# Kernel optimization log

Hardware: AMD Instinct MI355X
Metric: run time of the kernel (lower is better)

## Reference

```python
import jax, jax.numpy as jnp
import numpy as np

L = 256
UP = 2
# ktype -> (rotations, ((pad_top,pad_bot),(pad_left,pad_right)), (b_row_off, b_col_off))
CONFIG = {
    'h': ([0, 2],        ((0, 0), (0, 1)), (0, 1)),
    'd': ([0, 1, 2, 3],  ((0, 1), (0, 1)), (1, 1)),
    'v': ([0, 2],        ((0, 1), (0, 0)), (1, 0)),
}


def setup_inputs() -> dict:
    key = jax.random.key(0)
    k0, k1, k2, k3 = jax.random.split(key, 4)
    img_lr = jax.random.randint(k0, (32, 1, 512, 512), 0, L, dtype=jnp.int32)
    h_weight = jax.random.normal(k1, (L * L, UP * UP), dtype=jnp.float32)
    d_weight = jax.random.normal(k2, (L * L, UP * UP), dtype=jnp.float32)
    v_weight = jax.random.normal(k3, (L * L, UP * UP), dtype=jnp.float32)
    return {"img_lr": img_lr, "h_weight": h_weight, "d_weight": d_weight, "v_weight": v_weight}


def reference(img_lr, h_weight, d_weight, v_weight):
    B, C, H0, W0 = img_lr.shape
    weights = {'h': h_weight, 'd': d_weight, 'v': v_weight}
    out = jnp.zeros((B, C, H0 * UP, W0 * UP), dtype=jnp.float32)
    for ktype in ('h', 'd', 'v'):
        rots, (ph, pw), (dr, dc) = CONFIG[ktype]
        w = weights[ktype].reshape(L * L, UP, UP)
        for r in rots:
            rot = jnp.rot90(img_lr, r, axes=(2, 3))
            H, W = rot.shape[2], rot.shape[3]
            padded = jnp.pad(rot, ((0, 0), (0, 0), ph, pw), mode='edge').astype(jnp.int32)
            img_a = padded[:, :, 0:H, 0:W]
            img_b = padded[:, :, dr:dr + H, dc:dc + W]
            # LUT gather: [B,C,H,W,UP,UP]
            tmp = w[img_a * L + img_b]
            # interleave subpixels: (B,C,H,uh,W,uw) -> (B,C,H*UP,W*UP)
            tmp = tmp.transpose(0, 1, 2, 4, 3, 5).reshape(B, C, H * UP, W * UP)
            out = out + jnp.rot90(tmp, (4 - r) % 4, axes=(2, 3))
    return out / 2.0
```

## Files before the change

### kernel.cpp

```cpp
#include <hip/hip_runtime.h>


typedef _Float16 h8 __attribute__((ext_vector_type(8)));
typedef _Float16 h4 __attribute__((ext_vector_type(4)));
typedef unsigned u32x2 __attribute__((ext_vector_type(2)));
typedef float    f32x4 __attribute__((ext_vector_type(4)));

#define P3_CURS(ws, i) (((unsigned*)(ws))[(size_t)(i) << 4])
#define P3_LUT16(ws)   ((h4*)((char*)(ws) + 0x100000))
#define P3_SMAP(ws)    ((unsigned*)((char*)(ws) + 0x280000))
#define P3_RECS(ws)    ((u32x2*)((char*)(ws) + 0x2280000))
#define P3_RES(ws)     ((h4*)((char*)(ws) + 0x8280000))
#define P3_AB(ws)      ((unsigned char*)((char*)(ws) + 0xE280000))
#define P3_NEED        0xEE80000ull
#define P3_CAP         12288u

__global__ __launch_bounds__(256) void p3_init(void* ws)
{
    for (int k = 0; k < 4; ++k) {
        int i = k * 256 + threadIdx.x;
        if (i < 1024) P3_CURS(ws, i) = (unsigned)i * P3_CAP;
    }
}

__global__ __launch_bounds__(256) void p2_lut16(
    const float4* __restrict__ wh,
    const float4* __restrict__ wv,
    const float4* __restrict__ wd,
    h4* __restrict__ lut16)
{
    int idx = blockIdx.x * 256 + threadIdx.x;
    int l = idx >> 16, pq = idx & 65535;
    const float4* src = (l == 0) ? wh : (l == 1) ? wv : wd;
    float4 f = src[pq];
    h4 e;
    e[0] = (_Float16)f.x; e[1] = (_Float16)f.y;
    e[2] = (_Float16)f.z; e[3] = (_Float16)f.w;
    lut16[idx] = e;
}

__global__ __launch_bounds__(256) void p3_sort(
    const int* __restrict__ img, void* ws)
{
    __shared__ int stage[66 * 66];
    __shared__ unsigned lh[32], lbase[32], lcur[32];
    int t = threadIdx.x;
    int blk = blockIdx.x;
    int imgb = blk >> 6;
    int tile = blk & 63;
    int oy = (tile >> 3) << 6, ox = (tile & 7) << 6;
    const int* I = img + ((size_t)imgb << 18);

    for (int l = t; l < 4356; l += 256) {
        int ly = l / 66, lx = l - ly * 66;
        int gy = oy + ly - 1; gy = (gy < 0) ? 0 : (gy > 511 ? 511 : gy);
        int gx = ox + lx - 1; gx = (gx < 0) ? 0 : (gx > 511 ? 511 : gx);
        stage[l] = I[(gy << 9) + gx];
    }
    if (t < 32) { lh[t] = 0u; lcur[t] = 0u; }
    __syncthreads();

    for (int k = 0; k < 16; ++k) {
        int l = k * 256 + t;
        int ci = ((l >> 6) + 1) * 66 + (l & 63) + 1;
        atomicAdd(&lh[((unsigned)stage[ci]) >> 3], 1u);
    }
    __syncthreads();
    if (t < 32 && lh[t]) lbase[t] = atomicAdd(&P3_CURS(ws, imgb * 32 + t), lh[t]);
    __syncthreads();

    u32x2* RECS = P3_RECS(ws);
    unsigned char* AB = P3_AB(ws);
    unsigned* SMAP = P3_SMAP(ws) + (size_t)imgb * 262144;
    for (int k = 0; k < 16; ++k) {
        int l = k * 256 + t;
        int ly = l >> 6, lx = l & 63;
        int ci = (ly + 1) * 66 + lx + 1;
        unsigned a  = (unsigned)stage[ci];
        unsigned E  = (unsigned)stage[ci + 1],  W_ = (unsigned)stage[ci - 1];
        unsigned S  = (unsigned)stage[ci + 66], N_ = (unsigned)stage[ci - 66];
        unsigned SE = (unsigned)stage[ci + 67], SW = (unsigned)stage[ci + 65];
        unsigned NW = (unsigned)stage[ci - 67], NE = (unsigned)stage[ci - 65];
        unsigned g = a >> 3;
        unsigned slot = lbase[g] + atomicAdd(&lcur[g], 1u);
        u32x2 r;
        r[0] = E  | (W_ << 8) | (S  << 16) | (N_ << 24);
        r[1] = SE | (SW << 8) | (NW << 16) | (NE << 24);
        RECS[slot] = r;
        AB[slot] = (unsigned char)(a & 7u);
        SMAP[((oy + ly) << 9) + ox + lx] = slot;
    }
}

__global__ __launch_bounds__(256) void p3_compute(
    const h4* __restrict__ LUT16, void* ws)
{
    __shared__ h4 sh[3][8][256];
    int t = threadIdx.x;
    int bid = blockIdx.x;
    int imgb = bid / 96;
    int r = bid - imgb * 96;
    int g = r / 3, c = r - (r / 3) * 3;
    unsigned base = (unsigned)(imgb * 32 + g) * P3_CAP;
    unsigned endv = P3_CURS(ws, imgb * 32 + g);
    unsigned start = base + (unsigned)c * 4096u;
    if (start >= endv) return;

    for (int l = 0; l < 3; ++l)
        for (int j = 0; j < 8; ++j)
            sh[l][j][t] = LUT16[l * 65536 + ((g * 8 + j) << 8) + t];
    __syncthreads();

    u32x2* RECS = P3_RECS(ws);
    h4* RES = P3_RES(ws);
    const unsigned char* AB = P3_AB(ws);
    for (int k = 0; k < 16; ++k) {
        unsigned slot = start + (unsigned)k * 256u + (unsigned)t;
        if (slot >= endv) break;
        u32x2 rec = __builtin_nontemporal_load(&RECS[slot]);
        int j = AB[slot];
        unsigned n0 = rec[0], n1 = rec[1];
        h4 t4; float ax, ay, az, aw;
        t4 = sh[0][j][n0 & 255];         ax  = (float)t4[0]; ay  = (float)t4[1]; az  = (float)t4[2]; aw  = (float)t4[3];
        t4 = sh[0][j][(n0 >> 8) & 255];  ax += (float)t4[3]; ay += (float)t4[2]; az += (float)t4[1]; aw += (float)t4[0];
        t4 = sh[1][j][(n0 >> 16) & 255]; ax += (float)t4[0]; ay += (float)t4[1]; az += (float)t4[2]; aw += (float)t4[3];
        t4 = sh[1][j][n0 >> 24];         ax += (float)t4[3]; ay += (float)t4[2]; az += (float)t4[1]; aw += (float)t4[0];
        t4 = sh[2][j][n1 & 255];         ax += (float)t4[0]; ay += (float)t4[1]; az += (float)t4[2]; aw += (float)t4[3];
        t4 = sh[2][j][(n1 >> 8) & 255];  ax += (float)t4[2]; ay += (float)t4[0]; az += (float)t4[3]; aw += (float)t4[1];
        t4 = sh[2][j][(n1 >> 16) & 255]; ax += (float)t4[3]; ay += (float)t4[2]; az += (float)t4[1]; aw += (float)t4[0];
        t4 = sh[2][j][n1 >> 24];         ax += (float)t4[1]; ay += (float)t4[3]; az += (float)t4[0]; aw += (float)t4[2];
        h4 res;
        res[0] = (_Float16)(ax * 0.5f); res[1] = (_Float16)(ay * 0.5f);
        res[2] = (_Float16)(az * 0.5f); res[3] = (_Float16)(aw * 0.5f);
        RES[slot] = res;
    }
}

__global__ __launch_bounds__(256) void p3_unsort(
    void* ws, float* __restrict__ out)
{
    int bid = blockIdx.x;
    int xcd = bid & 7;
    int rest = bid >> 3;
    int imgb = xcd * 4 + (rest >> 7);
    int within = rest & 127;
    int t = threadIdx.x;
    const unsigned* SM = P3_SMAP(ws) + (size_t)imgb * 262144;
    const h4* RES = P3_RES(ws);
    for (int k = 0; k < 4; ++k) {
        int pair = within * 1024 + k * 256 + t;
        int p = pair << 1;
        u32x2 ss = *(const u32x2*)(SM + p);
        h4 r0 = RES[ss[0]];
        h4 r1 = RES[ss[1]];
        int x = p & 511, y = p >> 9;
        size_t obase = ((((size_t)imgb << 10) + (size_t)(y << 1)) << 10) + (size_t)(x << 1);
        f32x4 row0, row1;
        row0[0] = (float)r0[0]; row0[1] = (float)r0[1];
        row0[2] = (float)r1[0]; row0[3] = (float)r1[1];
        row1[0] = (float)r0[2]; row1[1] = (float)r0[3];
        row1[2] = (float)r1[2]; row1[3] = (float)r1[3];
        __builtin_nontemporal_store(row0, (f32x4*)(out + obase));
        __builtin_nontemporal_store(row1, (f32x4*)(out + obase + 1024));
    }
}

__global__ __launch_bounds__(256) void hdvlut_prep(
    const float4* __restrict__ wh,
    const float4* __restrict__ wd,
    const float4* __restrict__ wv,
    h8* __restrict__ ws)
{
    int idx = blockIdx.x * 256 + threadIdx.x;
    int lut = idx >> 16;
    int pq  = idx & 65535;
    int p = pq >> 8, q = pq & 255;
    const float4* src = (lut == 0) ? wh : (lut == 1) ? wv : wd;
    float4 f = src[pq];
    float4 g = src[(q << 8) | p];
    h8 e;
    e[0] = (_Float16)f.x; e[1] = (_Float16)f.y;
    e[2] = (_Float16)f.z; e[3] = (_Float16)f.w;
    e[4] = (_Float16)g.x; e[5] = (_Float16)g.y;
    e[6] = (_Float16)g.z; e[7] = (_Float16)g.w;
    ws[idx] = e;
}

__global__ __launch_bounds__(256) void hdvlut_merged(
    const int* __restrict__ img,
    const h8* __restrict__ W2,
    float* __restrict__ out)
{
    __shared__ h4 bwdE[256], bwdS[256], bwdSE[256], bwdSW[256];

    int t  = threadIdx.x;
    int tx = t & 15, ty = t >> 4;
    int blk   = blockIdx.x;
    int tileX = blk & 31;
    int tileY = (blk >> 5) & 31;
    int b     = blk >> 10;
    int x = (tileX << 4) | tx;
    int y = (tileY << 4) | ty;

    const int* I = img + ((size_t)b << 18);

    int xm = (x > 0)   ? x - 1 : 0;
    int xp = (x < 511) ? x + 1 : 511;
    int ym = (y > 0)   ? y - 1 : 0;
    int yp = (y < 511) ? y + 1 : 511;
    int rM = y << 9, rN = ym << 9, rS = yp << 9;

    int a   = I[rM + x];
    int aE  = I[rM + xp], aW  = I[rM + xm];
    int aS  = I[rS + x ], aN  = I[rN + x ];
    int aSE = I[rS + xp], aSW = I[rS + xm];
    int aNW = I[rN + xm], aNE = I[rN + xp];
    int aL = a << 8;

    const h8* H2 = W2;
    const h8* V2 = W2 + 65536;
    const h8* D2 = W2 + 131072;

    h8 fE  = H2[aL + aE ];
    h8 fS  = V2[aL + aS ];
    h8 fSE = D2[aL + aSE];
    h8 fSW = D2[aL + aSW];

    bool bW  = (tx == 0);
    bool bN  = (ty == 0);
    bool bNW = bN || bW;
    bool bNE = bN || (tx == 15);
    h8 dW = {}, dN = {}, dNW = {}, dNE = {};
    if (bW)  dW  = H2[aL + aW ];
    if (bN)  dN  = V2[aL + aN ];
    if (bNW) dNW = D2[aL + aNW];
    if (bNE) dNE = D2[aL + aNE];

    bwdE [t] = __builtin_shufflevector(fE,  fE,  4, 5, 6, 7);
    bwdS [t] = __builtin_shufflevector(fS,  fS,  4, 5, 6, 7);
    bwdSE[t] = __builtin_shufflevector(fSE, fSE, 4, 5, 6, 7);
    bwdSW[t] = __builtin_shufflevector(fSW, fSW, 4, 5, 6, 7);
    __syncthreads();

    int txm = (tx > 0)  ? tx - 1 : 0;
    int txp = (tx < 15) ? tx + 1 : 15;
    int tym = (ty > 0)  ? ty - 1 : 0;
    h4 lW  = bwdE [(ty  << 4) | txm];
    h4 lN  = bwdS [(tym << 4) | tx ];
    h4 lNW = bwdSE[(tym << 4) | txm];
    h4 lNE = bwdSW[(tym << 4) | txp];

    h4 vW  = bW  ? __builtin_shufflevector(dW,  dW,  0, 1, 2, 3) : lW;
    h4 vN  = bN  ? __builtin_shufflevector(dN,  dN,  0, 1, 2, 3) : lN;
    h4 vNW = bNW ? __builtin_shufflevector(dNW, dNW, 0, 1, 2, 3) : lNW;
    h4 vNE = bNE ? __builtin_shufflevector(dNE, dNE, 0, 1, 2, 3) : lNE;

    float ax, ay, az, aw;
    ax  = (float)fE[0];  ay  = (float)fE[1];  az  = (float)fE[2];  aw  = (float)fE[3];
    ax += (float)fS[0];  ay += (float)fS[1];  az += (float)fS[2];  aw += (float)fS[3];
    ax += (float)fSE[0]; ay += (float)fSE[1]; az += (float)fSE[2]; aw += (float)fSE[3];
    ax += (float)fSW[2]; ay += (float)fSW[0]; az += (float)fSW[3]; aw += (float)fSW[1];
    ax += (float)vW[3];  ay += (float)vW[2];  az += (float)vW[1];  aw += (float)vW[0];
    ax += (float)vN[3];  ay += (float)vN[2];  az += (float)vN[1];  aw += (float)vN[0];
    ax += (float)vNW[3]; ay += (float)vNW[2]; az += (float)vNW[1]; aw += (float)vNW[0];
    ax += (float)vNE[1]; ay += (float)vNE[3]; az += (float)vNE[0]; aw += (float)vNE[2];

    size_t obase = ((((size_t)b << 10) + (y << 1)) << 10) + (x << 1);
    *(float2*)(out + obase)        = make_float2(ax * 0.5f, ay * 0.5f);
    *(float2*)(out + obase + 1024) = make_float2(az * 0.5f, aw * 0.5f);
}

__global__ __launch_bounds__(256) void hdvlut_plain(
    const int* __restrict__ img,
    const float4* __restrict__ wh,
    const float4* __restrict__ wd,
    const float4* __restrict__ wv,
    float* __restrict__ out)
{
    int idx = blockIdx.x * 256 + threadIdx.x;
    int x = idx & 511, y = (idx >> 9) & 511, b = idx >> 18;
    const int* I = img + ((size_t)b << 18);
    int row = y << 9;
    int xm = (x > 0) ? x - 1 : 0, xp = (x < 511) ? x + 1 : 511;
    int ym = (y > 0) ? y - 1 : 0, yp = (y < 511) ? y + 1 : 511;
    int rN = ym << 9, rS = yp << 9;
    int a = I[row|x], E = I[row|xp], W_ = I[row|xm], S = I[rS|x], N_ = I[rN|x];
    int SE = I[rS|xp], SW = I[rS|xm], NW = I[rN|xm], NE = I[rN|xp];
    int aL = a << 8;
    float4 t; float ax, ay, az, aw;
    t = wh[aL+E ]; ax  = t.x; ay  = t.y; az  = t.z; aw  = t.w;
    t = wh[aL+W_]; ax += t.w; ay += t.z; az += t.y; aw += t.x;
    t = wv[aL+S ]; ax += t.x; ay += t.y; az += t.z; aw += t.w;
    t = wv[aL+N_]; ax += t.w; ay += t.z; az += t.y; aw += t.x;
    t = wd[aL+SE]; ax += t.x; ay += t.y; az += t.z; aw += t.w;
    t = wd[aL+SW]; ax += t.z; ay += t.x; az += t.w; aw += t.y;
    t = wd[aL+NW]; ax += t.w; ay += t.z; az += t.y; aw += t.x;
    t = wd[aL+NE]; ax += t.y; ay += t.w; az += t.x; aw += t.z;
    size_t obase = ((((size_t)b << 10) + (y << 1)) << 10) + (x << 1);
    *(float2*)(out + obase)        = make_float2(ax*0.5f, ay*0.5f);
    *(float2*)(out + obase + 1024) = make_float2(az*0.5f, aw*0.5f);
}

extern "C" void kernel_launch(void* const* d_in, const int* in_sizes, int n_in,
                              void* d_out, int out_size, void* d_ws, size_t ws_size,
                              hipStream_t stream) {
    const int*    img = (const int*)d_in[0];
    const float4* wh  = (const float4*)d_in[1];
    const float4* wd  = (const float4*)d_in[2];
    const float4* wv  = (const float4*)d_in[3];
    float* out = (float*)d_out;

    int total = in_sizes[0];
    size_t need_merged = (size_t)3 * 65536 * 16;

    if (ws_size >= P3_NEED && (total >> 18) == 32) {
        hipLaunchKernelGGL(p3_init,    dim3(1),    dim3(256), 0, stream, d_ws);
        hipLaunchKernelGGL(p2_lut16,   dim3(768),  dim3(256), 0, stream,
                           wh, wv, wd, P3_LUT16(d_ws));
        hipLaunchKernelGGL(p3_sort,    dim3(2048), dim3(256), 0, stream,
                           img, d_ws);
        hipLaunchKernelGGL(p3_compute, dim3(3072), dim3(256), 0, stream,
                           P3_LUT16(d_ws), d_ws);
        hipLaunchKernelGGL(p3_unsort,  dim3(4096), dim3(256), 0, stream,
                           d_ws, out);
    } else if (ws_size >= need_merged) {
        h8* W2 = (h8*)d_ws;
        hipLaunchKernelGGL(hdvlut_prep, dim3(768), dim3(256), 0, stream,
                           wh, wd, wv, W2);
        hipLaunchKernelGGL(hdvlut_merged, dim3(total / 256), dim3(256), 0, stream,
                           img, W2, out);
    } else {
        hipLaunchKernelGGL(hdvlut_plain, dim3(total / 256), dim3(256), 0, stream,
                           img, wh, wd, wv, out);
    }
}
```

Before: 274.9 us.

## Bucket pixels by exact LUT row and shrink per-block LUT tile

The sort pass now buckets pixels by their full 8-bit centre value (256 buckets per image) instead of 32 groups of 8. This removes the per-record subgroup byte array and shrinks each compute block's shared LUT tile from 48KB to 6KB, which should raise occupancy. The compute kernel processes two records per thread using 16-byte loads and 16-byte half-precision stores. Counter initialisation is folded into the LUT conversion kernel, saving one launch. In exchange there are more, smaller buckets and more global atomics, and the fixed per-bucket capacity of 2048 assumes the pixel values are roughly uniform.

```diff
diff --git a/kernel.cpp b/kernel.cpp
--- a/kernel.cpp
+++ b/kernel.cpp
@@ -4,46 +4,42 @@
 typedef _Float16 h8 __attribute__((ext_vector_type(8)));
 typedef _Float16 h4 __attribute__((ext_vector_type(4)));
 typedef unsigned u32x2 __attribute__((ext_vector_type(2)));
+typedef unsigned u32x4 __attribute__((ext_vector_type(4)));
 typedef float    f32x4 __attribute__((ext_vector_type(4)));
 
-#define P3_CURS(ws, i) (((unsigned*)(ws))[(size_t)(i) << 4])
-#define P3_LUT16(ws)   ((h4*)((char*)(ws) + 0x100000))
-#define P3_SMAP(ws)    ((unsigned*)((char*)(ws) + 0x280000))
-#define P3_RECS(ws)    ((u32x2*)((char*)(ws) + 0x2280000))
-#define P3_RES(ws)     ((h4*)((char*)(ws) + 0x8280000))
-#define P3_AB(ws)      ((unsigned char*)((char*)(ws) + 0xE280000))
-#define P3_NEED        0xEE80000ull
-#define P3_CAP         12288u
-
-__global__ __launch_bounds__(256) void p3_init(void* ws)
-{
-    for (int k = 0; k < 4; ++k) {
-        int i = k * 256 + threadIdx.x;
-        if (i < 1024) P3_CURS(ws, i) = (unsigned)i * P3_CAP;
-    }
-}
-
-__global__ __launch_bounds__(256) void p2_lut16(
+#define P4_CURS(ws, i) (((unsigned*)(ws))[(size_t)(i) << 4])
+#define P4_LUT16(ws)   ((h4*)((char*)(ws) + 0x80000))
+#define P4_SMAP(ws)    ((unsigned*)((char*)(ws) + 0x200000))
+#define P4_RECS(ws)    ((u32x2*)((char*)(ws) + 0x2200000))
+#define P4_RES(ws)     ((h4*)((char*)(ws) + 0xA200000))
+#define P4_NEED        0x12200000ull
+#define P4_CAP         2048u
+
+__global__ __launch_bounds__(256) void p4_lut16(
     const float4* __restrict__ wh,
     const float4* __restrict__ wv,
     const float4* __restrict__ wd,
-    h4* __restrict__ lut16)
+    void* ws)
 {
     int idx = blockIdx.x * 256 + threadIdx.x;
+    if (blockIdx.x < 32) {
+        int i = blockIdx.x * 256 + threadIdx.x;
+        P4_CURS(ws, i) = (unsigned)i * P4_CAP;
+    }
     int l = idx >> 16, pq = idx & 65535;
     const float4* src = (l == 0) ? wh : (l == 1) ? wv : wd;
     float4 f = src[pq];
     h4 e;
     e[0] = (_Float16)f.x; e[1] = (_Float16)f.y;
     e[2] = (_Float16)f.z; e[3] = (_Float16)f.w;
-    lut16[idx] = e;
-}
-
-__global__ __launch_bounds__(256) void p3_sort(
+    P4_LUT16(ws)[idx] = e;
+}
+
+__global__ __launch_bounds__(256) void p4_sort(
     const int* __restrict__ img, void* ws)
 {
     __shared__ int stage[66 * 66];
-    __shared__ unsigned lh[32], lbase[32], lcur[32];
+    __shared__ unsigned lh[256], lbase[256], lcur[256];
     int t = threadIdx.x;
     int blk = blockIdx.x;
     int imgb = blk >> 6;
@@ -57,21 +53,20 @@
         int gx = ox + lx - 1; gx = (gx < 0) ? 0 : (gx > 511 ? 511 : gx);
         stage[l] = I[(gy << 9) + gx];
     }
-    if (t < 32) { lh[t] = 0u; lcur[t] = 0u; }
+    lh[t] = 0u; lcur[t] = 0u;
     __syncthreads();
 
     for (int k = 0; k < 16; ++k) {
         int l = k * 256 + t;
         int ci = ((l >> 6) + 1) * 66 + (l & 63) + 1;
-        atomicAdd(&lh[((unsigned)stage[ci]) >> 3], 1u);
-    }
-    __syncthreads();
-    if (t < 32 && lh[t]) lbase[t] = atomicAdd(&P3_CURS(ws, imgb * 32 + t), lh[t]);
-    __syncthreads();
-
-    u32x2* RECS = P3_RECS(ws);
-    unsigned char* AB = P3_AB(ws);
-    unsigned* SMAP = P3_SMAP(ws) + (size_t)imgb * 262144;
+        atomicAdd(&lh[(unsigned)stage[ci]], 1u);
+    }
+    __syncthreads();
+    if (lh[t]) lbase[t] = atomicAdd(&P4_CURS(ws, imgb * 256 + t), lh[t]);
+    __syncthreads();
+
+    u32x2* RECS = P4_RECS(ws);
+    unsigned* SMAP = P4_SMAP(ws) + (size_t)imgb * 262144;
     for (int k = 0; k < 16; ++k) {
         int l = k * 256 + t;
         int ly = l >> 6, lx = l & 63;
@@ -81,62 +76,73 @@
         unsigned S  = (unsigned)stage[ci + 66], N_ = (unsigned)stage[ci - 66];
         unsigned SE = (unsigned)stage[ci + 67], SW = (unsigned)stage[ci + 65];
         unsigned NW = (unsigned)stage[ci - 67], NE = (unsigned)stage[ci - 65];
-        unsigned g = a >> 3;
-        unsigned slot = lbase[g] + atomicAdd(&lcur[g], 1u);
+        unsigned slot = lbase[a] + atomicAdd(&lcur[a], 1u);
         u32x2 r;
         r[0] = E  | (W_ << 8) | (S  << 16) | (N_ << 24);
         r[1] = SE | (SW << 8) | (NW << 16) | (NE << 24);
         RECS[slot] = r;
-        AB[slot] = (unsigned char)(a & 7u);
         SMAP[((oy + ly) << 9) + ox + lx] = slot;
     }
 }
 
-__global__ __launch_bounds__(256) void p3_compute(
-    const h4* __restrict__ LUT16, void* ws)
-{
-    __shared__ h4 sh[3][8][256];
+__global__ __launch_bounds__(256) void p4_compute(void* ws)
+{
+    __shared__ h4 sh[3][256];
     int t = threadIdx.x;
     int bid = blockIdx.x;
-    int imgb = bid / 96;
-    int r = bid - imgb * 96;
-    int g = r / 3, c = r - (r / 3) * 3;
-    unsigned base = (unsigned)(imgb * 32 + g) * P3_CAP;
-    unsigned endv = P3_CURS(ws, imgb * 32 + g);
-    unsigned start = base + (unsigned)c * 4096u;
-    if (start >= endv) return;
-
-    for (int l = 0; l < 3; ++l)
-        for (int j = 0; j < 8; ++j)
-            sh[l][j][t] = LUT16[l * 65536 + ((g * 8 + j) << 8) + t];
-    __syncthreads();
-
-    u32x2* RECS = P3_RECS(ws);
-    h4* RES = P3_RES(ws);
-    const unsigned char* AB = P3_AB(ws);
-    for (int k = 0; k < 16; ++k) {
-        unsigned slot = start + (unsigned)k * 256u + (unsigned)t;
-        if (slot >= endv) break;
-        u32x2 rec = __builtin_nontemporal_load(&RECS[slot]);
-        int j = AB[slot];
-        unsigned n0 = rec[0], n1 = rec[1];
-        h4 t4; float ax, ay, az, aw;
-        t4 = sh[0][j][n0 & 255];         ax  = (float)t4[0]; ay  = (float)t4[1]; az  = (float)t4[2]; aw  = (float)t4[3];
-        t4 = sh[0][j][(n0 >> 8) & 255];  ax += (float)t4[3]; ay += (float)t4[2]; az += (float)t4[1]; aw += (float)t4[0];
-        t4 = sh[1][j][(n0 >> 16) & 255]; ax += (float)t4[0]; ay += (float)t4[1]; az += (float)t4[2]; aw += (float)t4[3];
-        t4 = sh[1][j][n0 >> 24];         ax += (float)t4[3]; ay += (float)t4[2]; az += (float)t4[1]; aw += (float)t4[0];
-        t4 = sh[2][j][n1 & 255];         ax += (float)t4[0]; ay += (float)t4[1]; az += (float)t4[2]; aw += (float)t4[3];
-        t4 = sh[2][j][(n1 >> 8) & 255];  ax += (float)t4[2]; ay += (float)t4[0]; az += (float)t4[3]; aw += (float)t4[1];
-        t4 = sh[2][j][(n1 >> 16) & 255]; ax += (float)t4[3]; ay += (float)t4[2]; az += (float)t4[1]; aw += (float)t4[0];
-        t4 = sh[2][j][n1 >> 24];         ax += (float)t4[1]; ay += (float)t4[3]; az += (float)t4[0]; aw += (float)t4[2];
-        h4 res;
-        res[0] = (_Float16)(ax * 0.5f); res[1] = (_Float16)(ay * 0.5f);
-        res[2] = (_Float16)(az * 0.5f); res[3] = (_Float16)(aw * 0.5f);
-        RES[slot] = res;
-    }
-}
-
-__global__ __launch_bounds__(256) void p3_unsort(
+    int v = bid & 255;
+    unsigned base = (unsigned)bid * P4_CAP;
+    unsigned endv = P4_CURS(ws, bid);
+    if (base >= endv) return;
+
+    const h4* LUT16 = P4_LUT16(ws);
+    sh[0][t] = LUT16[(v << 8) + t];
+    sh[1][t] = LUT16[65536 + (v << 8) + t];
+    sh[2][t] = LUT16[131072 + (v << 8) + t];
+    __syncthreads();
+
+    u32x2* RECS = P4_RECS(ws);
+    h4* RES = P4_RES(ws);
+    for (int k = 0; k < 4; ++k) {
+        unsigned s0 = base + (((unsigned)k * 256u + (unsigned)t) << 1);
+        if (s0 >= endv) break;
+        u32x4 rr = __builtin_nontemporal_load((const u32x4*)(RECS + s0));
+        h4 t4; float ax, ay, az, aw, bx, by, bz, bw;
+        unsigned n0 = rr[0], n1 = rr[1];
+        t4 = sh[0][n0 & 255];         ax  = (float)t4[0]; ay  = (float)t4[1]; az  = (float)t4[2]; aw  = (float)t4[3];
+        t4 = sh[0][(n0 >> 8) & 255];  ax += (float)t4[3]; ay += (float)t4[2]; az += (float)t4[1]; aw += (float)t4[0];
+        t4 = sh[1][(n0 >> 16) & 255]; ax += (float)t4[0]; ay += (float)t4[1]; az += (float)t4[2]; aw += (float)t4[3];
+        t4 = sh[1][n0 >> 24];         ax += (float)t4[3]; ay += (float)t4[2]; az += (float)t4[1]; aw += (float)t4[0];
+        t4 = sh[2][n1 & 255];         ax += (float)t4[0]; ay += (float)t4[1]; az += (float)t4[2]; aw += (float)t4[3];
+        t4 = sh[2][(n1 >> 8) & 255];  ax += (float)t4[2]; ay += (float)t4[0]; az += (float)t4[3]; aw += (float)t4[1];
+        t4 = sh[2][(n1 >> 16) & 255]; ax += (float)t4[3]; ay += (float)t4[2]; az += (float)t4[1]; aw += (float)t4[0];
+        t4 = sh[2][n1 >> 24];         ax += (float)t4[1]; ay += (float)t4[3]; az += (float)t4[0]; aw += (float)t4[2];
+        unsigned m0 = rr[2], m1 = rr[3];
+        t4 = sh[0][m0 & 255];         bx  = (float)t4[0]; by  = (float)t4[1]; bz  = (float)t4[2]; bw  = (float)t4[3];
+        t4 = sh[0][(m0 >> 8) & 255];  bx += (float)t4[3]; by += (float)t4[2]; bz += (float)t4[1]; bw += (float)t4[0];
+        t4 = sh[1][(m0 >> 16) & 255]; bx += (float)t4[0]; by += (float)t4[1]; bz += (float)t4[2]; bw += (float)t4[3];
+        t4 = sh[1][m0 >> 24];         bx += (float)t4[3]; by += (float)t4[2]; bz += (float)t4[1]; bw += (float)t4[0];
+        t4 = sh[2][m1 & 255];         bx += (float)t4[0]; by += (float)t4[1]; bz += (float)t4[2]; bw += (float)t4[3];
+        t4 = sh[2][(m1 >> 8) & 255];  bx += (float)t4[2]; by += (float)t4[0]; bz += (float)t4[3]; bw += (float)t4[1];
+        t4 = sh[2][(m1 >> 16) & 255]; bx += (float)t4[3]; by += (float)t4[2]; bz += (float)t4[1]; bw += (float)t4[0];
+        t4 = sh[2][m1 >> 24];         bx += (float)t4[1]; by += (float)t4[3]; bz += (float)t4[0]; bw += (float)t4[2];
+        if (s0 + 1 < endv) {
+            h8 pair;
+            pair[0] = (_Float16)(ax * 0.5f); pair[1] = (_Float16)(ay * 0.5f);
+            pair[2] = (_Float16)(az * 0.5f); pair[3] = (_Float16)(aw * 0.5f);
+            pair[4] = (_Float16)(bx * 0.5f); pair[5] = (_Float16)(by * 0.5f);
+            pair[6] = (_Float16)(bz * 0.5f); pair[7] = (_Float16)(bw * 0.5f);
+            __builtin_nontemporal_store(pair, (h8*)(RES + s0));
+        } else {
+            h4 res;
+            res[0] = (_Float16)(ax * 0.5f); res[1] = (_Float16)(ay * 0.5f);
+            res[2] = (_Float16)(az * 0.5f); res[3] = (_Float16)(aw * 0.5f);
+            RES[s0] = res;
+        }
+    }
+}
+
+__global__ __launch_bounds__(256) void p4_unsort(
     void* ws, float* __restrict__ out)
 {
     int bid = blockIdx.x;
@@ -145,8 +151,8 @@
     int imgb = xcd * 4 + (rest >> 7);
     int within = rest & 127;
     int t = threadIdx.x;
-    const unsigned* SM = P3_SMAP(ws) + (size_t)imgb * 262144;
-    const h4* RES = P3_RES(ws);
+    const unsigned* SM = P4_SMAP(ws) + (size_t)imgb * 262144;
+    const h4* RES = P4_RES(ws);
     for (int k = 0; k < 4; ++k) {
         int pair = within * 1024 + k * 256 + t;
         int p = pair << 1;
@@ -313,15 +319,14 @@
     int total = in_sizes[0];
     size_t need_merged = (size_t)3 * 65536 * 16;
 
-    if (ws_size >= P3_NEED && (total >> 18) == 32) {
-        hipLaunchKernelGGL(p3_init,    dim3(1),    dim3(256), 0, stream, d_ws);
-        hipLaunchKernelGGL(p2_lut16,   dim3(768),  dim3(256), 0, stream,
-                           wh, wv, wd, P3_LUT16(d_ws));
-        hipLaunchKernelGGL(p3_sort,    dim3(2048), dim3(256), 0, stream,
+    if (ws_size >= P4_NEED && (total >> 18) == 32) {
+        hipLaunchKernelGGL(p4_lut16,   dim3(768),  dim3(256), 0, stream,
+                           wh, wv, wd, d_ws);
+        hipLaunchKernelGGL(p4_sort,    dim3(2048), dim3(256), 0, stream,
                            img, d_ws);
-        hipLaunchKernelGGL(p3_compute, dim3(3072), dim3(256), 0, stream,
-                           P3_LUT16(d_ws), d_ws);
-        hipLaunchKernelGGL(p3_unsort,  dim3(4096), dim3(256), 0, stream,
+        hipLaunchKernelGGL(p4_compute, dim3(8192), dim3(256), 0, stream,
+                           d_ws);
+        hipLaunchKernelGGL(p4_unsort,  dim3(4096), dim3(256), 0, stream,
                            d_ws, out);
     } else if (ws_size >= need_merged) {
         h8* W2 = (h8*)d_ws;
```

Result: slower. 322.8 us (+17.4%).
